# Kernel tuning notes

Measured on AMD Instinct MI355X. Metric: run time of the kernel, lower is better.

The kernel has to match this reference:

```python
import jax, jax.numpy as jnp
import numpy as np

N_NODES = 100000
N_EDGES = 3200000
N_GRAPHS = 128
IN_DIM, HID, OUT = 128, 64, 128


def gcn_conv(x, W, b, src, dst, n_nodes):
    """PyG GCNConv: add self-loops, symmetric deg^-1/2 normalization, scatter-add."""
    xw = x @ W  # [N, H]
    ones = jnp.ones(src.shape[0], dtype=x.dtype)
    deg = jax.ops.segment_sum(ones, dst, num_segments=n_nodes) + 1.0  # +1 self loop
    dinv = jax.lax.rsqrt(deg)
    norm = dinv[src] * dinv[dst]  # [E]
    agg = jax.ops.segment_sum(xw[src] * norm[:, None], dst, num_segments=n_nodes)
    # self-loop contribution: norm = dinv * dinv = 1/deg
    return agg + xw * (1.0 / deg)[:, None] + b


def global_mean_pool(x, batch, n_graphs):
    sums = jax.ops.segment_sum(x, batch, num_segments=n_graphs)
    cnts = jax.ops.segment_sum(jnp.ones(x.shape[0], dtype=x.dtype), batch, num_segments=n_graphs)
    return sums / jnp.maximum(cnts, 1.0)[:, None]


def setup_inputs() -> dict:
    key = jax.random.key(0)
    ks = jax.random.split(key, 9)
    x = jax.random.normal(ks[0], (N_NODES, IN_DIM), dtype=jnp.float32)
    edge_index = jax.random.randint(ks[1], (2, N_EDGES), 0, N_NODES, dtype=jnp.int64)
    batch = jnp.sort(jax.random.randint(ks[2], (N_NODES,), 0, N_GRAPHS, dtype=jnp.int64))
    def glorot(k, shp):
        lim = float(np.sqrt(6.0 / (shp[0] + shp[1])))
        return jax.random.uniform(k, shp, dtype=jnp.float32, minval=-lim, maxval=lim)
    return {
        "x": x,
        "edge_index": edge_index,
        "batch": batch,
        "W1": glorot(ks[3], (IN_DIM, HID)),
        "b1": jnp.zeros((HID,), jnp.float32),
        "W2": glorot(ks[4], (HID, HID)),
        "b2": jnp.zeros((HID,), jnp.float32),
        "Wl": glorot(ks[5], (HID, OUT)),
        "bl": jnp.zeros((OUT,), jnp.float32),
    }


def reference(x, edge_index, batch, W1, b1, W2, b2, Wl, bl):
    src, dst = edge_index[0], edge_index[1]
    h = jax.nn.relu(gcn_conv(x, W1, b1, src, dst, N_NODES))
    h = jax.nn.relu(gcn_conv(h, W2, b2, src, dst, N_NODES))
    g = global_mean_pool(h, batch, N_GRAPHS)  # [G, HID]
    return g @ Wl + bl  # [G, OUT]
```

## Files before the change

### kernel.cpp

```cpp
#include <hip/hip_runtime.h>
#include <math.h>

#define N_NODES    100000
#define N_EDGES    3200000
#define N_GRAPHS   128
#define IN_DIM     128
#define HID        64
#define OUT_DIM    128
#define NSUP       98
#define SUP_SHIFT  10
#define SUP_MASK   1023
#define BIN_BLOCKS 512
#define E_PER_BIN  6250

typedef unsigned short ushort_t;

__device__ __forceinline__ ushort_t f2bf(float f) {
    unsigned int u = __float_as_uint(f);
    u += 0x7FFFu + ((u >> 16) & 1u);
    return (ushort_t)(u >> 16);
}

__global__ __launch_bounds__(256) void k_hist(const int* __restrict__ dst,
                                              int* __restrict__ sup_cnt,
                                              int* __restrict__ hist_mat) {
    __shared__ int hist[NSUP];
    int t = threadIdx.x;
    if (t < NSUP) hist[t] = 0;
    __syncthreads();
    int e0 = blockIdx.x * E_PER_BIN;
    for (int e = e0 + t; e < e0 + E_PER_BIN; e += 256)
        atomicAdd(&hist[dst[e] >> SUP_SHIFT], 1);
    __syncthreads();
    if (t < NSUP) {
        int h = hist[t];
        hist_mat[blockIdx.x * NSUP + t] = h;
        if (h) atomicAdd(&sup_cnt[t], h);
    }
}

__global__ void k_scan_sup(const int* __restrict__ sup_cnt,
                           int* __restrict__ sup_ptr, int* __restrict__ sup_cur) {
    __shared__ int s[128];
    int t = threadIdx.x;
    int v = (t < NSUP) ? sup_cnt[t] : 0;
    s[t] = v; __syncthreads();
    for (int d = 1; d < 128; d <<= 1) {
        int add = (t >= d) ? s[t - d] : 0;
        __syncthreads();
        s[t] += add;
        __syncthreads();
    }
    int excl = s[t] - v;
    if (t <= NSUP) sup_ptr[t] = excl;
    if (t < NSUP)  sup_cur[t] = excl;
}

__global__ __launch_bounds__(256) void k_super(const int* __restrict__ src,
                                               const int* __restrict__ dst,
                                               const int* __restrict__ hist_mat,
                                               int* __restrict__ sup_cursor,
                                               unsigned int* __restrict__ recs) {
    __shared__ int base[NSUP];
    __shared__ int hist[NSUP];
    int t = threadIdx.x;
    int e0 = blockIdx.x * E_PER_BIN;
    if (t < NSUP) {
        int h = hist_mat[blockIdx.x * NSUP + t];
        base[t] = h ? atomicAdd(&sup_cursor[t], h) : 0;
        hist[t] = 0;
    }
    __syncthreads();
    for (int e = e0 + t; e < e0 + E_PER_BIN; e += 256) {
        int d = dst[e];
        int b = d >> SUP_SHIFT;
        int pos = base[b] + atomicAdd(&hist[b], 1);
        recs[pos] = ((unsigned int)src[e] << SUP_SHIFT) | (unsigned int)(d & SUP_MASK);
    }
}

__global__ __launch_bounds__(1024) void k_csrB(const unsigned int* __restrict__ recs,
                                               const int* __restrict__ sup_ptr,
                                               int* __restrict__ row_ptr,
                                               float* __restrict__ dinv,
                                               int* __restrict__ csr_src) {
    __shared__ int lcnt[1024];
    __shared__ int s[1024];
    __shared__ int lcur[1024];
    int b = blockIdx.x, t = threadIdx.x;
    int start = sup_ptr[b], end = sup_ptr[b + 1];
    lcnt[t] = 0;
    __syncthreads();
    for (int i = start + t; i < end; i += 1024)
        atomicAdd(&lcnt[recs[i] & SUP_MASK], 1);
    __syncthreads();
    int v = lcnt[t];
    s[t] = v; __syncthreads();
    for (int d = 1; d < 1024; d <<= 1) {
        int add = (t >= d) ? s[t - d] : 0;
        __syncthreads();
        s[t] += add;
        __syncthreads();
    }
    int excl = s[t] - v;
    int n = b * 1024 + t;
    if (n <= N_NODES) row_ptr[n] = start + excl;
    if (n < N_NODES)  dinv[n] = 1.0f / sqrtf((float)v + 1.0f);
    lcur[t] = start + excl;
    __syncthreads();
    for (int i = start + t; i < end; i += 1024) {
        unsigned int r = recs[i];
        int p = atomicAdd(&lcur[r & SUP_MASK], 1);
        csr_src[p] = (int)(r >> SUP_SHIFT);
    }
}

template <int K>
__global__ __launch_bounds__(256) void k_gemm(const float* __restrict__ X,
                                              const float* __restrict__ W,
                                              const float* __restrict__ dinv,
                                              ushort_t* __restrict__ Ybf, int nrows) {
    __shared__ float Xs[64][65];
    __shared__ float Ws[64][64];
    int t = threadIdx.x;
    int row0 = blockIdx.x * 64;
    int tc = t & 15, tr = t >> 4;
    int c0 = tc * 4, r0 = tr * 4;
    float acc[4][4] = {};
    for (int kc = 0; kc < K; kc += 64) {
        __syncthreads();
#pragma unroll
        for (int i = 0; i < 16; ++i) {
            int e = i * 256 + t;
            int r = e >> 6, k = e & 63;
            int gr = row0 + r;
            Xs[r][k] = (gr < nrows) ? X[(size_t)gr * K + kc + k] : 0.0f;
        }
#pragma unroll
        for (int i = 0; i < 16; ++i) {
            int e = i * 256 + t;
            int k = e >> 6, c = e & 63;
            Ws[k][c] = W[(size_t)(kc + k) * 64 + c];
        }
        __syncthreads();
#pragma unroll 8
        for (int k = 0; k < 64; ++k) {
            float xv[4];
#pragma unroll
            for (int i = 0; i < 4; ++i) xv[i] = Xs[r0 + i][k];
            const float4 w4 = *(const float4*)&Ws[k][c0];
#pragma unroll
            for (int i = 0; i < 4; ++i) {
                acc[i][0] += xv[i] * w4.x;
                acc[i][1] += xv[i] * w4.y;
                acc[i][2] += xv[i] * w4.z;
                acc[i][3] += xv[i] * w4.w;
            }
        }
    }
#pragma unroll
    for (int i = 0; i < 4; ++i) {
        int gr = row0 + r0 + i;
        if (gr < nrows) {
            float dn = dinv[gr];
            ushort4 o;
            o.x = f2bf(dn * acc[i][0]);
            o.y = f2bf(dn * acc[i][1]);
            o.z = f2bf(dn * acc[i][2]);
            o.w = f2bf(dn * acc[i][3]);
            *(ushort4*)(Ybf + (size_t)gr * 64 + c0) = o;
        }
    }
}

__global__ __launch_bounds__(256) void k_gather(const ushort_t* __restrict__ xwp,
                                                const float* __restrict__ dinv,
                                                const int* __restrict__ row_ptr,
                                                const int* __restrict__ csr_src,
                                                const float* __restrict__ bias,
                                                float* __restrict__ hout) {
    int wave = threadIdx.x >> 6;
    int lane = threadIdx.x & 63;
    int n = blockIdx.x * 4 + wave;
    if (n >= N_NODES) return;
    int sub = lane >> 3, c8 = (lane & 7) * 8;
    int start = row_ptr[n], end = row_ptr[n + 1];
    double a[8] = {0.0, 0.0, 0.0, 0.0, 0.0, 0.0, 0.0, 0.0};
    int i = start + sub;
    for (; i + 8 < end; i += 16) {
        int s0 = csr_src[i];
        int s1 = csr_src[i + 8];
        const uint4 v0 = *(const uint4*)(xwp + (size_t)s0 * 64 + c8);
        const uint4 v1 = *(const uint4*)(xwp + (size_t)s1 * 64 + c8);
        a[0] += (double)__uint_as_float(v0.x << 16);
        a[1] += (double)__uint_as_float(v0.x & 0xFFFF0000u);
        a[2] += (double)__uint_as_float(v0.y << 16);
        a[3] += (double)__uint_as_float(v0.y & 0xFFFF0000u);
        a[4] += (double)__uint_as_float(v0.z << 16);
        a[5] += (double)__uint_as_float(v0.z & 0xFFFF0000u);
        a[6] += (double)__uint_as_float(v0.w << 16);
        a[7] += (double)__uint_as_float(v0.w & 0xFFFF0000u);
        a[0] += (double)__uint_as_float(v1.x << 16);
        a[1] += (double)__uint_as_float(v1.x & 0xFFFF0000u);
        a[2] += (double)__uint_as_float(v1.y << 16);
        a[3] += (double)__uint_as_float(v1.y & 0xFFFF0000u);
        a[4] += (double)__uint_as_float(v1.z << 16);
        a[5] += (double)__uint_as_float(v1.z & 0xFFFF0000u);
        a[6] += (double)__uint_as_float(v1.w << 16);
        a[7] += (double)__uint_as_float(v1.w & 0xFFFF0000u);
    }
    if (i < end) {
        int s0 = csr_src[i];
        const uint4 v = *(const uint4*)(xwp + (size_t)s0 * 64 + c8);
        a[0] += (double)__uint_as_float(v.x << 16);
        a[1] += (double)__uint_as_float(v.x & 0xFFFF0000u);
        a[2] += (double)__uint_as_float(v.y << 16);
        a[3] += (double)__uint_as_float(v.y & 0xFFFF0000u);
        a[4] += (double)__uint_as_float(v.z << 16);
        a[5] += (double)__uint_as_float(v.z & 0xFFFF0000u);
        a[6] += (double)__uint_as_float(v.w << 16);
        a[7] += (double)__uint_as_float(v.w & 0xFFFF0000u);
    }
#pragma unroll
    for (int off = 8; off < 64; off <<= 1) {
#pragma unroll
        for (int j = 0; j < 8; ++j) a[j] += __shfl_xor(a[j], off, 64);
    }
    if (sub == 0) {
        float dn = dinv[n];
        const uint4 xn = *(const uint4*)(xwp + (size_t)n * 64 + c8);
        float xnf[8];
        xnf[0] = __uint_as_float(xn.x << 16); xnf[1] = __uint_as_float(xn.x & 0xFFFF0000u);
        xnf[2] = __uint_as_float(xn.y << 16); xnf[3] = __uint_as_float(xn.y & 0xFFFF0000u);
        xnf[4] = __uint_as_float(xn.z << 16); xnf[5] = __uint_as_float(xn.z & 0xFFFF0000u);
        xnf[6] = __uint_as_float(xn.w << 16); xnf[7] = __uint_as_float(xn.w & 0xFFFF0000u);
        float4 b0 = *(const float4*)(bias + c8);
        float4 b1 = *(const float4*)(bias + c8 + 4);
        float4 r0, r1;
        r0.x = fmaxf(dn * ((float)a[0] + xnf[0]) + b0.x, 0.f);
        r0.y = fmaxf(dn * ((float)a[1] + xnf[1]) + b0.y, 0.f);
        r0.z = fmaxf(dn * ((float)a[2] + xnf[2]) + b0.z, 0.f);
        r0.w = fmaxf(dn * ((float)a[3] + xnf[3]) + b0.w, 0.f);
        r1.x = fmaxf(dn * ((float)a[4] + xnf[4]) + b1.x, 0.f);
        r1.y = fmaxf(dn * ((float)a[5] + xnf[5]) + b1.y, 0.f);
        r1.z = fmaxf(dn * ((float)a[6] + xnf[6]) + b1.z, 0.f);
        r1.w = fmaxf(dn * ((float)a[7] + xnf[7]) + b1.w, 0.f);
        *(float4*)(hout + (size_t)n * 64 + c8)     = r0;
        *(float4*)(hout + (size_t)n * 64 + c8 + 4) = r1;
    }
}

__device__ __forceinline__ int lower_bound(const int* __restrict__ a, int n, int key) {
    int lo = 0, hi = n;
    while (lo < hi) {
        int mid = (lo + hi) >> 1;
        if (a[mid] < key) lo = mid + 1; else hi = mid;
    }
    return lo;
}

__global__ __launch_bounds__(1024) void k_poolfinal(const float* __restrict__ h,
                                                    const int* __restrict__ batch,
                                                    const float* __restrict__ Wl,
                                                    const float* __restrict__ bl,
                                                    float* __restrict__ out) {
    int b = blockIdx.x;
    int t = threadIdx.x, c = t & 63, rg = t >> 6;
    __shared__ float s[16][64];
    __shared__ float gs[64];
    int start = lower_bound(batch, N_NODES, b);
    int end   = lower_bound(batch, N_NODES, b + 1);
    float sum = 0.f;
    for (int n = start + rg; n < end; n += 16) sum += h[(size_t)n * 64 + c];
    s[rg][c] = sum;
    __syncthreads();
    if (rg == 0) {
        float tot = 0.f;
#pragma unroll
        for (int k = 0; k < 16; ++k) tot += s[k][c];
        gs[c] = tot / fmaxf((float)(end - start), 1.0f);
    }
    __syncthreads();
    if (t < 128) {
        float acc = bl[t];
#pragma unroll
        for (int k = 0; k < 64; ++k) acc += gs[k] * Wl[k * 128 + t];
        out[b * 128 + t] = acc;
    }
}

extern "C" void kernel_launch(void* const* d_in, const int* in_sizes, int n_in,
                              void* d_out, int out_size, void* d_ws, size_t ws_size,
                              hipStream_t stream) {
    const float* x    = (const float*)d_in[0];
    const int*   ei   = (const int*)d_in[1];
    const int*   batch= (const int*)d_in[2];
    const float* W1   = (const float*)d_in[3];
    const float* b1   = (const float*)d_in[4];
    const float* W2   = (const float*)d_in[5];
    const float* b2   = (const float*)d_in[6];
    const float* Wl   = (const float*)d_in[7];
    const float* bl   = (const float*)d_in[8];
    float* out = (float*)d_out;

    const int* src = ei;
    const int* dst = ei + N_EDGES;

    char* base = (char*)d_ws;
    float*        dinv     = (float*)(base + 0);
    int*          row_ptr  = (int*)  (base + 400128);
    int*          sup_cnt  = (int*)  (base + 800256);
    int*          sup_ptr  = (int*)  (base + 802304);
    int*          sup_cur  = (int*)  (base + 804352);
    int*          hist_mat = (int*)  (base + 806400);
    int*          csr_src  = (int*)  (base + 1007616);
    ushort_t*     xwp      = (ushort_t*)(base + 13807616);
    float*        h        = (float*)(base + 26607616);
    unsigned int* recs     = (unsigned int*)xwp;

    hipMemsetAsync(sup_cnt, 0, NSUP * sizeof(int), stream);
    k_hist    <<<BIN_BLOCKS, 256, 0, stream>>>(dst, sup_cnt, hist_mat);
    k_scan_sup<<<1, 128, 0, stream>>>(sup_cnt, sup_ptr, sup_cur);
    k_super   <<<BIN_BLOCKS, 256, 0, stream>>>(src, dst, hist_mat, sup_cur, recs);
    k_csrB    <<<NSUP, 1024, 0, stream>>>(recs, sup_ptr, row_ptr, dinv, csr_src);

    const int GEMM_GRID = (N_NODES + 63) / 64;

    k_gemm<IN_DIM><<<GEMM_GRID, 256, 0, stream>>>(x, W1, dinv, xwp, N_NODES);
    k_gather<<<(N_NODES + 3) / 4, 256, 0, stream>>>(xwp, dinv, row_ptr, csr_src, b1, h);

    k_gemm<HID><<<GEMM_GRID, 256, 0, stream>>>(h, W2, dinv, xwp, N_NODES);
    k_gather<<<(N_NODES + 3) / 4, 256, 0, stream>>>(xwp, dinv, row_ptr, csr_src, b2, h);

    k_poolfinal<<<N_GRAPHS, 1024, 0, stream>>>(h, batch, Wl, bl, out);
}
```

Before: 314.0 us.

## Fuse CSR preprocessing kernels into one cooperative kernel with grid syncs

Merges the memset, histogram, super-bin scan, scatter and per-bin CSR build kernels into a single cooperative launch separated by grid.sync barriers. The aim is to cut the launch overhead and inter-kernel gaps of the preprocessing chain. The CSR phase now runs with 256 threads per block instead of 1024, each thread handling four nodes in the scan. This adds grid-wide barrier cost, serial column summation in block 0, and less parallelism in the CSR build stage.

```diff
diff --git a/kernel.cpp b/kernel.cpp
--- a/kernel.cpp
+++ b/kernel.cpp
@@ -1,5 +1,8 @@
 #include <hip/hip_runtime.h>
+#include <hip/hip_cooperative_groups.h>
 #include <math.h>
+
+namespace cg = cooperative_groups;
 
 #define N_NODES    100000
 #define N_EDGES    3200000
@@ -21,97 +24,99 @@
     return (ushort_t)(u >> 16);
 }
 
-__global__ __launch_bounds__(256) void k_hist(const int* __restrict__ dst,
-                                              int* __restrict__ sup_cnt,
-                                              int* __restrict__ hist_mat) {
-    __shared__ int hist[NSUP];
-    int t = threadIdx.x;
-    if (t < NSUP) hist[t] = 0;
-    __syncthreads();
-    int e0 = blockIdx.x * E_PER_BIN;
+__global__ __launch_bounds__(256, 2) void k_preproc(
+        const int* __restrict__ src, const int* __restrict__ dst,
+        int* __restrict__ hist_mat, int* __restrict__ sup_ptr,
+        int* __restrict__ sup_cur, unsigned int* __restrict__ recs,
+        int* __restrict__ row_ptr, float* __restrict__ dinv,
+        int* __restrict__ csr_src) {
+    cg::grid_group grid = cg::this_grid();
+    __shared__ int lcnt[1024];
+    __shared__ int lcur[1024];
+    __shared__ int s2[256];
+    int t = threadIdx.x, bid = blockIdx.x;
+    int e0 = bid * E_PER_BIN;
+
+    if (t < NSUP) lcnt[t] = 0;
+    __syncthreads();
     for (int e = e0 + t; e < e0 + E_PER_BIN; e += 256)
-        atomicAdd(&hist[dst[e] >> SUP_SHIFT], 1);
-    __syncthreads();
+        atomicAdd(&lcnt[dst[e] >> SUP_SHIFT], 1);
+    __syncthreads();
+    if (t < NSUP) hist_mat[bid * NSUP + t] = lcnt[t];
+    grid.sync();
+
+    int colsum = 0;
+    if (bid == 0) {
+        if (t < NSUP) {
+#pragma unroll 8
+            for (int r = 0; r < BIN_BLOCKS; ++r) colsum += hist_mat[r * NSUP + t];
+        }
+        s2[t] = (t < NSUP) ? colsum : 0;
+        __syncthreads();
+        for (int d = 1; d < 128; d <<= 1) {
+            int add = (t < 128 && t >= d) ? s2[t - d] : 0;
+            __syncthreads();
+            if (t < 128) s2[t] += add;
+            __syncthreads();
+        }
+        if (t < 128) {
+            int excl = s2[t] - ((t < NSUP) ? colsum : 0);
+            if (t <= NSUP) sup_ptr[t] = excl;
+            if (t < NSUP)  sup_cur[t] = excl;
+        }
+    }
+    grid.sync();
+
     if (t < NSUP) {
-        int h = hist[t];
-        hist_mat[blockIdx.x * NSUP + t] = h;
-        if (h) atomicAdd(&sup_cnt[t], h);
-    }
-}
-
-__global__ void k_scan_sup(const int* __restrict__ sup_cnt,
-                           int* __restrict__ sup_ptr, int* __restrict__ sup_cur) {
-    __shared__ int s[128];
-    int t = threadIdx.x;
-    int v = (t < NSUP) ? sup_cnt[t] : 0;
-    s[t] = v; __syncthreads();
-    for (int d = 1; d < 128; d <<= 1) {
-        int add = (t >= d) ? s[t - d] : 0;
-        __syncthreads();
-        s[t] += add;
-        __syncthreads();
-    }
-    int excl = s[t] - v;
-    if (t <= NSUP) sup_ptr[t] = excl;
-    if (t < NSUP)  sup_cur[t] = excl;
-}
-
-__global__ __launch_bounds__(256) void k_super(const int* __restrict__ src,
-                                               const int* __restrict__ dst,
-                                               const int* __restrict__ hist_mat,
-                                               int* __restrict__ sup_cursor,
-                                               unsigned int* __restrict__ recs) {
-    __shared__ int base[NSUP];
-    __shared__ int hist[NSUP];
-    int t = threadIdx.x;
-    int e0 = blockIdx.x * E_PER_BIN;
-    if (t < NSUP) {
-        int h = hist_mat[blockIdx.x * NSUP + t];
-        base[t] = h ? atomicAdd(&sup_cursor[t], h) : 0;
-        hist[t] = 0;
+        int h = hist_mat[bid * NSUP + t];
+        lcur[t] = h ? atomicAdd(&sup_cur[t], h) : 0;
+        lcnt[t] = 0;
     }
     __syncthreads();
     for (int e = e0 + t; e < e0 + E_PER_BIN; e += 256) {
         int d = dst[e];
         int b = d >> SUP_SHIFT;
-        int pos = base[b] + atomicAdd(&hist[b], 1);
+        int pos = lcur[b] + atomicAdd(&lcnt[b], 1);
         recs[pos] = ((unsigned int)src[e] << SUP_SHIFT) | (unsigned int)(d & SUP_MASK);
     }
-}
-
-__global__ __launch_bounds__(1024) void k_csrB(const unsigned int* __restrict__ recs,
-                                               const int* __restrict__ sup_ptr,
-                                               int* __restrict__ row_ptr,
-                                               float* __restrict__ dinv,
-                                               int* __restrict__ csr_src) {
-    __shared__ int lcnt[1024];
-    __shared__ int s[1024];
-    __shared__ int lcur[1024];
-    int b = blockIdx.x, t = threadIdx.x;
-    int start = sup_ptr[b], end = sup_ptr[b + 1];
-    lcnt[t] = 0;
-    __syncthreads();
-    for (int i = start + t; i < end; i += 1024)
-        atomicAdd(&lcnt[recs[i] & SUP_MASK], 1);
-    __syncthreads();
-    int v = lcnt[t];
-    s[t] = v; __syncthreads();
-    for (int d = 1; d < 1024; d <<= 1) {
-        int add = (t >= d) ? s[t - d] : 0;
-        __syncthreads();
-        s[t] += add;
-        __syncthreads();
-    }
-    int excl = s[t] - v;
-    int n = b * 1024 + t;
-    if (n <= N_NODES) row_ptr[n] = start + excl;
-    if (n < N_NODES)  dinv[n] = 1.0f / sqrtf((float)v + 1.0f);
-    lcur[t] = start + excl;
-    __syncthreads();
-    for (int i = start + t; i < end; i += 1024) {
-        unsigned int r = recs[i];
-        int p = atomicAdd(&lcur[r & SUP_MASK], 1);
-        csr_src[p] = (int)(r >> SUP_SHIFT);
+    grid.sync();
+
+    if (bid < NSUP) {
+        int start = sup_ptr[bid], end = sup_ptr[bid + 1];
+        for (int k = t; k < 1024; k += 256) lcnt[k] = 0;
+        __syncthreads();
+        for (int i = start + t; i < end; i += 256)
+            atomicAdd(&lcnt[recs[i] & SUP_MASK], 1);
+        __syncthreads();
+        int c0 = lcnt[t * 4], c1 = lcnt[t * 4 + 1];
+        int c2 = lcnt[t * 4 + 2], c3 = lcnt[t * 4 + 3];
+        int tsum = c0 + c1 + c2 + c3;
+        s2[t] = tsum;
+        __syncthreads();
+        for (int d = 1; d < 256; d <<= 1) {
+            int add = (t >= d) ? s2[t - d] : 0;
+            __syncthreads();
+            s2[t] += add;
+            __syncthreads();
+        }
+        int texcl = s2[t] - tsum;
+        int off[4];
+        off[0] = texcl; off[1] = off[0] + c0; off[2] = off[1] + c1; off[3] = off[2] + c2;
+        int cnts[4] = {c0, c1, c2, c3};
+        int nb = bid * 1024;
+#pragma unroll
+        for (int j = 0; j < 4; ++j) {
+            int n = nb + t * 4 + j;
+            if (n <= N_NODES) row_ptr[n] = start + off[j];
+            if (n < N_NODES)  dinv[n] = 1.0f / sqrtf((float)cnts[j] + 1.0f);
+            lcur[t * 4 + j] = start + off[j];
+        }
+        __syncthreads();
+        for (int i = start + t; i < end; i += 256) {
+            unsigned int r = recs[i];
+            int p = atomicAdd(&lcur[r & SUP_MASK], 1);
+            csr_src[p] = (int)(r >> SUP_SHIFT);
+        }
     }
 }
 
@@ -309,20 +314,21 @@
     char* base = (char*)d_ws;
     float*        dinv     = (float*)(base + 0);
     int*          row_ptr  = (int*)  (base + 400128);
-    int*          sup_cnt  = (int*)  (base + 800256);
-    int*          sup_ptr  = (int*)  (base + 802304);
-    int*          sup_cur  = (int*)  (base + 804352);
-    int*          hist_mat = (int*)  (base + 806400);
-    int*          csr_src  = (int*)  (base + 1007616);
-    ushort_t*     xwp      = (ushort_t*)(base + 13807616);
-    float*        h        = (float*)(base + 26607616);
+    int*          sup_ptr  = (int*)  (base + 800256);
+    int*          sup_cur  = (int*)  (base + 802304);
+    int*          hist_mat = (int*)  (base + 804352);
+    int*          csr_src  = (int*)  (base + 1005568);
+    ushort_t*     xwp      = (ushort_t*)(base + 13805568);
+    float*        h        = (float*)(base + 26605568);
     unsigned int* recs     = (unsigned int*)xwp;
 
-    hipMemsetAsync(sup_cnt, 0, NSUP * sizeof(int), stream);
-    k_hist    <<<BIN_BLOCKS, 256, 0, stream>>>(dst, sup_cnt, hist_mat);
-    k_scan_sup<<<1, 128, 0, stream>>>(sup_cnt, sup_ptr, sup_cur);
-    k_super   <<<BIN_BLOCKS, 256, 0, stream>>>(src, dst, hist_mat, sup_cur, recs);
-    k_csrB    <<<NSUP, 1024, 0, stream>>>(recs, sup_ptr, row_ptr, dinv, csr_src);
+    void* pp_args[] = {
+        (void*)&src, (void*)&dst, (void*)&hist_mat, (void*)&sup_ptr,
+        (void*)&sup_cur, (void*)&recs, (void*)&row_ptr, (void*)&dinv,
+        (void*)&csr_src
+    };
+    hipLaunchCooperativeKernel((void*)k_preproc, dim3(BIN_BLOCKS), dim3(256),
+                               pp_args, 0, stream);
 
     const int GEMM_GRID = (N_NODES + 63) / 64;
 
```

After: 521.6 us. 66.1% more time.

## Fuse histogram and scatter into single pass with fixed-capacity super-bins

Applied to the files above, without the earlier changes.

Merges the edge histogram and super-bin scatter kernels into one kernel. Each block counts its edges per super-bin, reserves space in a fixed-capacity per-bin region with a global atomic, then scatters records. The scan now runs after placement and only supplies CSR output offsets. This drops one pass over dst and the hist_mat traffic, plus one launch. It assumes no super-bin exceeds CAP records (about 33k expected per bin), which holds for uniform random input but would overflow on skewed graphs.

```diff
diff --git a/kernel.cpp b/kernel.cpp
--- a/kernel.cpp
+++ b/kernel.cpp
@@ -12,6 +12,7 @@
 #define SUP_MASK   1023
 #define BIN_BLOCKS 512
 #define E_PER_BIN  6250
+#define CAP        36864
 
 typedef unsigned short ushort_t;
 
@@ -21,29 +22,39 @@
     return (ushort_t)(u >> 16);
 }
 
-__global__ __launch_bounds__(256) void k_hist(const int* __restrict__ dst,
-                                              int* __restrict__ sup_cnt,
-                                              int* __restrict__ hist_mat) {
-    __shared__ int hist[NSUP];
+__global__ __launch_bounds__(256) void k_place(const int* __restrict__ src,
+                                               const int* __restrict__ dst,
+                                               int* __restrict__ sup_cur,
+                                               unsigned int* __restrict__ recs) {
+    __shared__ int cnt[NSUP];
+    __shared__ int base[NSUP];
     int t = threadIdx.x;
-    if (t < NSUP) hist[t] = 0;
-    __syncthreads();
     int e0 = blockIdx.x * E_PER_BIN;
+    if (t < NSUP) cnt[t] = 0;
+    __syncthreads();
     for (int e = e0 + t; e < e0 + E_PER_BIN; e += 256)
-        atomicAdd(&hist[dst[e] >> SUP_SHIFT], 1);
+        atomicAdd(&cnt[dst[e] >> SUP_SHIFT], 1);
     __syncthreads();
     if (t < NSUP) {
-        int h = hist[t];
-        hist_mat[blockIdx.x * NSUP + t] = h;
-        if (h) atomicAdd(&sup_cnt[t], h);
-    }
-}
-
-__global__ void k_scan_sup(const int* __restrict__ sup_cnt,
-                           int* __restrict__ sup_ptr, int* __restrict__ sup_cur) {
+        int h = cnt[t];
+        base[t] = h ? atomicAdd(&sup_cur[t], h) : 0;
+        cnt[t] = 0;
+    }
+    __syncthreads();
+    for (int e = e0 + t; e < e0 + E_PER_BIN; e += 256) {
+        int d = dst[e];
+        int b = d >> SUP_SHIFT;
+        int pos = base[b] + atomicAdd(&cnt[b], 1);
+        recs[(size_t)b * CAP + pos] =
+            ((unsigned int)src[e] << SUP_SHIFT) | (unsigned int)(d & SUP_MASK);
+    }
+}
+
+__global__ void k_scan_sup(const int* __restrict__ sup_cur,
+                           int* __restrict__ sup_ptr) {
     __shared__ int s[128];
     int t = threadIdx.x;
-    int v = (t < NSUP) ? sup_cnt[t] : 0;
+    int v = (t < NSUP) ? sup_cur[t] : 0;
     s[t] = v; __syncthreads();
     for (int d = 1; d < 128; d <<= 1) {
         int add = (t >= d) ? s[t - d] : 0;
@@ -53,30 +64,6 @@
     }
     int excl = s[t] - v;
     if (t <= NSUP) sup_ptr[t] = excl;
-    if (t < NSUP)  sup_cur[t] = excl;
-}
-
-__global__ __launch_bounds__(256) void k_super(const int* __restrict__ src,
-                                               const int* __restrict__ dst,
-                                               const int* __restrict__ hist_mat,
-                                               int* __restrict__ sup_cursor,
-                                               unsigned int* __restrict__ recs) {
-    __shared__ int base[NSUP];
-    __shared__ int hist[NSUP];
-    int t = threadIdx.x;
-    int e0 = blockIdx.x * E_PER_BIN;
-    if (t < NSUP) {
-        int h = hist_mat[blockIdx.x * NSUP + t];
-        base[t] = h ? atomicAdd(&sup_cursor[t], h) : 0;
-        hist[t] = 0;
-    }
-    __syncthreads();
-    for (int e = e0 + t; e < e0 + E_PER_BIN; e += 256) {
-        int d = dst[e];
-        int b = d >> SUP_SHIFT;
-        int pos = base[b] + atomicAdd(&hist[b], 1);
-        recs[pos] = ((unsigned int)src[e] << SUP_SHIFT) | (unsigned int)(d & SUP_MASK);
-    }
 }
 
 __global__ __launch_bounds__(1024) void k_csrB(const unsigned int* __restrict__ recs,
@@ -88,11 +75,13 @@
     __shared__ int s[1024];
     __shared__ int lcur[1024];
     int b = blockIdx.x, t = threadIdx.x;
-    int start = sup_ptr[b], end = sup_ptr[b + 1];
+    int out0 = sup_ptr[b];
+    int cnt  = sup_ptr[b + 1] - out0;
+    const unsigned int* rbase = recs + (size_t)b * CAP;
     lcnt[t] = 0;
     __syncthreads();
-    for (int i = start + t; i < end; i += 1024)
-        atomicAdd(&lcnt[recs[i] & SUP_MASK], 1);
+    for (int i = t; i < cnt; i += 1024)
+        atomicAdd(&lcnt[rbase[i] & SUP_MASK], 1);
     __syncthreads();
     int v = lcnt[t];
     s[t] = v; __syncthreads();
@@ -104,12 +93,12 @@
     }
     int excl = s[t] - v;
     int n = b * 1024 + t;
-    if (n <= N_NODES) row_ptr[n] = start + excl;
+    if (n <= N_NODES) row_ptr[n] = out0 + excl;
     if (n < N_NODES)  dinv[n] = 1.0f / sqrtf((float)v + 1.0f);
-    lcur[t] = start + excl;
-    __syncthreads();
-    for (int i = start + t; i < end; i += 1024) {
-        unsigned int r = recs[i];
+    lcur[t] = out0 + excl;
+    __syncthreads();
+    for (int i = t; i < cnt; i += 1024) {
+        unsigned int r = rbase[i];
         int p = atomicAdd(&lcur[r & SUP_MASK], 1);
         csr_src[p] = (int)(r >> SUP_SHIFT);
     }
@@ -309,19 +298,16 @@
     char* base = (char*)d_ws;
     float*        dinv     = (float*)(base + 0);
     int*          row_ptr  = (int*)  (base + 400128);
-    int*          sup_cnt  = (int*)  (base + 800256);
+    int*          sup_cur  = (int*)  (base + 800256);
     int*          sup_ptr  = (int*)  (base + 802304);
-    int*          sup_cur  = (int*)  (base + 804352);
-    int*          hist_mat = (int*)  (base + 806400);
-    int*          csr_src  = (int*)  (base + 1007616);
-    ushort_t*     xwp      = (ushort_t*)(base + 13807616);
-    float*        h        = (float*)(base + 26607616);
-    unsigned int* recs     = (unsigned int*)xwp;
-
-    hipMemsetAsync(sup_cnt, 0, NSUP * sizeof(int), stream);
-    k_hist    <<<BIN_BLOCKS, 256, 0, stream>>>(dst, sup_cnt, hist_mat);
-    k_scan_sup<<<1, 128, 0, stream>>>(sup_cnt, sup_ptr, sup_cur);
-    k_super   <<<BIN_BLOCKS, 256, 0, stream>>>(src, dst, hist_mat, sup_cur, recs);
+    int*          csr_src  = (int*)  (base + 804352);
+    ushort_t*     xwp      = (ushort_t*)(base + 13604352);
+    float*        h        = (float*)(base + 26404352);
+    unsigned int* recs     = (unsigned int*)h;
+
+    hipMemsetAsync(sup_cur, 0, NSUP * sizeof(int), stream);
+    k_place   <<<BIN_BLOCKS, 256, 0, stream>>>(src, dst, sup_cur, recs);
+    k_scan_sup<<<1, 128, 0, stream>>>(sup_cur, sup_ptr);
     k_csrB    <<<NSUP, 1024, 0, stream>>>(recs, sup_ptr, row_ptr, dinv, csr_src);
 
     const int GEMM_GRID = (N_NODES + 63) / 64;
```

New measurement: 300.9 us. 1.04x faster.
